# Kernel tuning notes

Hardware: AMD Instinct MI355X
Metric: run time of the kernel (lower is better)

Reference implementation:

```python
import jax, jax.numpy as jnp
import numpy as np


def _delta(x, window):
    # x: [B, T, D]; edge-replicate pad by `window` frames on each side,
    # then weighted antisymmetric finite difference: sum_j (x[t+j]-x[t-j])/(2j).
    B, T, D = x.shape
    pad = jnp.concatenate(
        [jnp.repeat(x[:, :1, :], window, axis=1), x, jnp.repeat(x[:, -1:, :], window, axis=1)],
        axis=1,
    )  # [B, T+2W, D]
    z = jnp.zeros_like(x)
    for j in range(1, window + 1):  # tiny fixed loop over window taps
        z = z + (pad[:, window + j: window + j + T, :] - pad[:, window - j: window - j + T, :]) / (2.0 * j)
    return z


def setup_inputs() -> dict:
    key = jax.random.key(0)
    inp = jax.random.normal(key, (32, 4096, 256), dtype=jnp.float32)
    return {"inp": inp, "window": 2}


def reference(inp, window):
    delta = _delta(inp, window)
    double_delta = _delta(delta, window)
    return jnp.concatenate([inp, delta, double_delta], axis=2)  # [B, T, 3D]
```

## Files before the change

### kernel.cpp

```cpp
#include <hip/hip_runtime.h>


#define TT   4096
#define D4   64
#define O4   192

__device__ __forceinline__ float4 dcomb(const float4 p1, const float4 m1,
                                        const float4 p2, const float4 m2) {
    float4 r;
    r.x = (p1.x - m1.x) * 0.5f + (p2.x - m2.x) * 0.25f;
    r.y = (p1.y - m1.y) * 0.5f + (p2.y - m2.y) * 0.25f;
    r.z = (p1.z - m1.z) * 0.5f + (p2.z - m2.z) * 0.25f;
    r.w = (p1.w - m1.w) * 0.5f + (p2.w - m2.w) * 0.25f;
    return r;
}

__device__ __forceinline__ int clampT(int s) {
    return s < 0 ? 0 : (s > TT - 1 ? TT - 1 : s);
}

__global__ __launch_bounds__(256) void delta_layer_kernel(
        const float* __restrict__ x, float* __restrict__ out) {
    int bid = blockIdx.x;
    int swz = (gridDim.x & 7) == 0
                  ? (bid & 7) * (gridDim.x >> 3) + (bid >> 3)
                  : bid;

    int idx = swz * 256 + (int)threadIdx.x;
    int d4  = idx & (D4 - 1);
    int g   = idx >> 6;
    int t   = g & (TT - 1);
    int b   = g >> 12;

    const float4* xr = reinterpret_cast<const float4*>(x)
                       + (size_t)g * D4 + d4;
    float4* ob = reinterpret_cast<float4*>(out)
                 + (size_t)g * O4 + d4;

    if (t >= 4 && t <= TT - 5) {
        float4 xm4 = xr[-4 * D4];
        float4 xm3 = xr[-3 * D4];
        float4 xm2 = xr[-2 * D4];
        float4 xm1 = xr[-1 * D4];
        float4 x0  = xr[0];
        float4 xp1 = xr[1 * D4];
        float4 xp2 = xr[2 * D4];
        float4 xp3 = xr[3 * D4];
        float4 xp4 = xr[4 * D4];

        float4 dm2 = dcomb(xm1, xm3, x0,  xm4);
        float4 dm1 = dcomb(x0,  xm2, xp1, xm3);
        float4 d0  = dcomb(xp1, xm1, xp2, xm2);
        float4 dp1 = dcomb(xp2, x0,  xp3, xm1);
        float4 dp2 = dcomb(xp3, xp1, xp4, x0);

        ob[0]      = x0;
        ob[D4]     = d0;
        ob[2 * D4] = dcomb(dp1, dm1, dp2, dm2);
    } else {
        const float4* xb = reinterpret_cast<const float4*>(x)
                           + (size_t)b * TT * D4 + d4;
        auto ldc = [&](int r) -> float4 { return xb[clampT(r) * D4]; };
        auto deltaAt = [&](int r) -> float4 {
            return dcomb(ldc(r + 1), ldc(r - 1), ldc(r + 2), ldc(r - 2));
        };
        float4 dm2 = deltaAt(clampT(t - 2));
        float4 dm1 = deltaAt(clampT(t - 1));
        float4 d0  = deltaAt(t);
        float4 dp1 = deltaAt(clampT(t + 1));
        float4 dp2 = deltaAt(clampT(t + 2));

        ob[0]      = ldc(t);
        ob[D4]     = d0;
        ob[2 * D4] = dcomb(dp1, dm1, dp2, dm2);
    }
}

extern "C" void kernel_launch(void* const* d_in, const int* in_sizes, int n_in,
                              void* d_out, int out_size, void* d_ws, size_t ws_size,
                              hipStream_t stream) {
    const float* x = (const float*)d_in[0];
    float* out = (float*)d_out;
    int nthreads = in_sizes[0] / 4;
    int blocks = (nthreads + 255) / 256;
    delta_layer_kernel<<<blocks, 256, 0, stream>>>(x, out);
}
```

Baseline: 515.4 us.

## Stage time-chunk halo tiles in shared memory and use nontemporal stores

Each block now handles a 32-row time chunk of one batch, loading the chunk plus a 4-row halo into LDS once, so the stencil reads come from shared memory rather than nine global reads per output row. Outputs are written with nontemporal stores to avoid polluting the cache with the write-only stream. The cost is an LDS barrier and fewer, larger blocks, with edge chunks still taking the clamped global path.

```diff
diff --git a/kernel.cpp b/kernel.cpp
--- a/kernel.cpp
+++ b/kernel.cpp
@@ -1,9 +1,20 @@
 #include <hip/hip_runtime.h>
 
 
-#define TT   4096
-#define D4   64
-#define O4   192
+#define TT     4096
+#define D4     64
+#define O4     192
+#define TCH    32
+#define NCH    (TT / TCH)
+#define SROWS  (TCH + 8)
+
+typedef float nfloat4 __attribute__((ext_vector_type(4)));
+
+__device__ __forceinline__ void ntstore(const float4 v, float4* p) {
+    union { float4 f; nfloat4 n; } u;
+    u.f = v;
+    __builtin_nontemporal_store(u.n, reinterpret_cast<nfloat4*>(p));
+}
 
 __device__ __forceinline__ float4 dcomb(const float4 p1, const float4 m1,
                                         const float4 p2, const float4 m2) {
@@ -21,58 +32,85 @@
 
 __global__ __launch_bounds__(256) void delta_layer_kernel(
         const float* __restrict__ x, float* __restrict__ out) {
+    __shared__ float4 sh[SROWS * D4];
+
     int bid = blockIdx.x;
     int swz = (gridDim.x & 7) == 0
                   ? (bid & 7) * (gridDim.x >> 3) + (bid >> 3)
                   : bid;
 
-    int idx = swz * 256 + (int)threadIdx.x;
-    int d4  = idx & (D4 - 1);
-    int g   = idx >> 6;
-    int t   = g & (TT - 1);
-    int b   = g >> 12;
+    int ct = swz & (NCH - 1);
+    int b  = swz >> 7;
+    int r0 = ct * TCH;
+    int tid = (int)threadIdx.x;
 
-    const float4* xr = reinterpret_cast<const float4*>(x)
-                       + (size_t)g * D4 + d4;
-    float4* ob = reinterpret_cast<float4*>(out)
-                 + (size_t)g * O4 + d4;
+    const float4* x4 = reinterpret_cast<const float4*>(x);
+    float4* out4 = reinterpret_cast<float4*>(out);
 
-    if (t >= 4 && t <= TT - 5) {
-        float4 xm4 = xr[-4 * D4];
-        float4 xm3 = xr[-3 * D4];
-        float4 xm2 = xr[-2 * D4];
-        float4 xm1 = xr[-1 * D4];
-        float4 x0  = xr[0];
-        float4 xp1 = xr[1 * D4];
-        float4 xp2 = xr[2 * D4];
-        float4 xp3 = xr[3 * D4];
-        float4 xp4 = xr[4 * D4];
+    if (ct >= 1 && ct <= NCH - 2) {
+        const float4* src = x4 + ((size_t)(b * TT + r0 - 4)) * D4;
+        #pragma unroll
+        for (int i = 0; i < SROWS * D4 / 256; ++i) {
+            int s = i * 256 + tid;
+            sh[s] = src[s];
+        }
+        __syncthreads();
 
-        float4 dm2 = dcomb(xm1, xm3, x0,  xm4);
-        float4 dm1 = dcomb(x0,  xm2, xp1, xm3);
-        float4 d0  = dcomb(xp1, xm1, xp2, xm2);
-        float4 dp1 = dcomb(xp2, x0,  xp3, xm1);
-        float4 dp2 = dcomb(xp3, xp1, xp4, x0);
+        #pragma unroll
+        for (int j = 0; j < 8; ++j) {
+            int o    = j * 256 + tid;
+            int trow = o >> 6;
+            int d4   = o & 63;
 
-        ob[0]      = x0;
-        ob[D4]     = d0;
-        ob[2 * D4] = dcomb(dp1, dm1, dp2, dm2);
+            const float4* L = &sh[trow * D4 + d4];
+            float4 xm4 = L[0 * D4];
+            float4 xm3 = L[1 * D4];
+            float4 xm2 = L[2 * D4];
+            float4 xm1 = L[3 * D4];
+            float4 x0  = L[4 * D4];
+            float4 xp1 = L[5 * D4];
+            float4 xp2 = L[6 * D4];
+            float4 xp3 = L[7 * D4];
+            float4 xp4 = L[8 * D4];
+
+            float4 dm2 = dcomb(xm1, xm3, x0,  xm4);
+            float4 dm1 = dcomb(x0,  xm2, xp1, xm3);
+            float4 d0  = dcomb(xp1, xm1, xp2, xm2);
+            float4 dp1 = dcomb(xp2, x0,  xp3, xm1);
+            float4 dp2 = dcomb(xp3, xp1, xp4, x0);
+            float4 dd  = dcomb(dp1, dm1, dp2, dm2);
+
+            float4* ob = out4 + ((size_t)(b * TT + r0 + trow)) * O4 + d4;
+            ntstore(x0, &ob[0]);
+            ntstore(d0, &ob[D4]);
+            ntstore(dd, &ob[2 * D4]);
+        }
     } else {
-        const float4* xb = reinterpret_cast<const float4*>(x)
-                           + (size_t)b * TT * D4 + d4;
-        auto ldc = [&](int r) -> float4 { return xb[clampT(r) * D4]; };
-        auto deltaAt = [&](int r) -> float4 {
-            return dcomb(ldc(r + 1), ldc(r - 1), ldc(r + 2), ldc(r - 2));
-        };
-        float4 dm2 = deltaAt(clampT(t - 2));
-        float4 dm1 = deltaAt(clampT(t - 1));
-        float4 d0  = deltaAt(t);
-        float4 dp1 = deltaAt(clampT(t + 1));
-        float4 dp2 = deltaAt(clampT(t + 2));
+        const float4* xb0 = x4 + (size_t)b * TT * D4;
+        #pragma unroll
+        for (int j = 0; j < 8; ++j) {
+            int o    = j * 256 + tid;
+            int trow = o >> 6;
+            int d4   = o & 63;
+            int t    = r0 + trow;
 
-        ob[0]      = ldc(t);
-        ob[D4]     = d0;
-        ob[2 * D4] = dcomb(dp1, dm1, dp2, dm2);
+            const float4* xb = xb0 + d4;
+            auto ldc = [&](int r) -> float4 { return xb[clampT(r) * D4]; };
+            auto deltaAt = [&](int r) -> float4 {
+                return dcomb(ldc(r + 1), ldc(r - 1), ldc(r + 2), ldc(r - 2));
+            };
+            float4 dm2 = deltaAt(clampT(t - 2));
+            float4 dm1 = deltaAt(clampT(t - 1));
+            float4 d0  = deltaAt(t);
+            float4 dp1 = deltaAt(clampT(t + 1));
+            float4 dp2 = deltaAt(clampT(t + 2));
+            float4 dd  = dcomb(dp1, dm1, dp2, dm2);
+
+            float4* ob = out4 + ((size_t)(b * TT + t)) * O4 + d4;
+            ntstore(ldc(t), &ob[0]);
+            ntstore(d0,     &ob[D4]);
+            ntstore(dd,     &ob[2 * D4]);
+        }
     }
 }
 
@@ -81,7 +119,7 @@
                               hipStream_t stream) {
     const float* x = (const float*)d_in[0];
     float* out = (float*)d_out;
-    int nthreads = in_sizes[0] / 4;
-    int blocks = (nthreads + 255) / 256;
+    int rows = in_sizes[0] / 256;
+    int blocks = rows / TCH;
     delta_layer_kernel<<<blocks, 256, 0, stream>>>(x, out);
 }
```

Measured after the change: 499.4 us. -3.1%, faster.

## Process 8-frame runs per thread with register reuse and nontemporal stores

Applied to the files above, without the earlier changes.

Each thread now computes eight consecutive time frames, loading a 16-frame window into registers once instead of nine loads per output frame. This cuts redundant global and L2 reads of the input. Output writes switch to nontemporal stores so the large output stream does not pollute the cache. The grid shrinks eightfold, which lowers occupancy and raises register pressure per thread.

```diff
diff --git a/kernel.cpp b/kernel.cpp
--- a/kernel.cpp
+++ b/kernel.cpp
@@ -1,9 +1,19 @@
 #include <hip/hip_runtime.h>
 
 
-#define TT   4096
-#define D4   64
-#define O4   192
+#define TT    4096
+#define D4    64
+#define O4    192
+#define WRUN  8
+#define SEGS  (TT / WRUN)
+
+typedef float nfloat4 __attribute__((ext_vector_type(4)));
+
+__device__ __forceinline__ void ntstore(const float4 v, float4* p) {
+    union { float4 f; nfloat4 n; } u;
+    u.f = v;
+    __builtin_nontemporal_store(u.n, reinterpret_cast<nfloat4*>(p));
+}
 
 __device__ __forceinline__ float4 dcomb(const float4 p1, const float4 m1,
                                         const float4 p2, const float4 m2) {
@@ -27,52 +37,55 @@
                   : bid;
 
     int idx = swz * 256 + (int)threadIdx.x;
-    int d4  = idx & (D4 - 1);
-    int g   = idx >> 6;
-    int t   = g & (TT - 1);
-    int b   = g >> 12;
+    int d4  = idx & 63;
+    int seg = idx >> 6;
+    int tb  = seg & (SEGS - 1);
+    int b   = seg >> 9;
+    int w0  = tb * WRUN;
 
-    const float4* xr = reinterpret_cast<const float4*>(x)
-                       + (size_t)g * D4 + d4;
-    float4* ob = reinterpret_cast<float4*>(out)
-                 + (size_t)g * O4 + d4;
+    const float4* x4 = reinterpret_cast<const float4*>(x);
+    float4* out4 = reinterpret_cast<float4*>(out);
 
-    if (t >= 4 && t <= TT - 5) {
-        float4 xm4 = xr[-4 * D4];
-        float4 xm3 = xr[-3 * D4];
-        float4 xm2 = xr[-2 * D4];
-        float4 xm1 = xr[-1 * D4];
-        float4 x0  = xr[0];
-        float4 xp1 = xr[1 * D4];
-        float4 xp2 = xr[2 * D4];
-        float4 xp3 = xr[3 * D4];
-        float4 xp4 = xr[4 * D4];
+    const float4* xr = x4 + ((size_t)(b * TT + w0)) * D4 + d4;
+    float4* ob = out4 + ((size_t)(b * TT + w0)) * O4 + d4;
 
-        float4 dm2 = dcomb(xm1, xm3, x0,  xm4);
-        float4 dm1 = dcomb(x0,  xm2, xp1, xm3);
-        float4 d0  = dcomb(xp1, xm1, xp2, xm2);
-        float4 dp1 = dcomb(xp2, x0,  xp3, xm1);
-        float4 dp2 = dcomb(xp3, xp1, xp4, x0);
+    if (w0 >= 4 && w0 + 11 <= TT - 1) {
+        float4 xq[16];
+        #pragma unroll
+        for (int i = 0; i < 16; ++i) xq[i] = xr[(i - 4) * D4];
 
-        ob[0]      = x0;
-        ob[D4]     = d0;
-        ob[2 * D4] = dcomb(dp1, dm1, dp2, dm2);
+        float4 d[12];
+        #pragma unroll
+        for (int j = 0; j < 12; ++j)
+            d[j] = dcomb(xq[j + 3], xq[j + 1], xq[j + 4], xq[j]);
+
+        #pragma unroll
+        for (int m = 0; m < 8; ++m) {
+            float4 dd = dcomb(d[m + 3], d[m + 1], d[m + 4], d[m]);
+            ntstore(xq[m + 4], &ob[m * O4]);
+            ntstore(d[m + 2],  &ob[m * O4 + D4]);
+            ntstore(dd,        &ob[m * O4 + 2 * D4]);
+        }
     } else {
-        const float4* xb = reinterpret_cast<const float4*>(x)
-                           + (size_t)b * TT * D4 + d4;
+        const float4* xb = x4 + (size_t)b * TT * D4 + d4;
         auto ldc = [&](int r) -> float4 { return xb[clampT(r) * D4]; };
         auto deltaAt = [&](int r) -> float4 {
             return dcomb(ldc(r + 1), ldc(r - 1), ldc(r + 2), ldc(r - 2));
         };
-        float4 dm2 = deltaAt(clampT(t - 2));
-        float4 dm1 = deltaAt(clampT(t - 1));
-        float4 d0  = deltaAt(t);
-        float4 dp1 = deltaAt(clampT(t + 1));
-        float4 dp2 = deltaAt(clampT(t + 2));
+        #pragma unroll
+        for (int m = 0; m < 8; ++m) {
+            int t = w0 + m;
+            float4 dm2 = deltaAt(clampT(t - 2));
+            float4 dm1 = deltaAt(clampT(t - 1));
+            float4 d0  = deltaAt(t);
+            float4 dp1 = deltaAt(clampT(t + 1));
+            float4 dp2 = deltaAt(clampT(t + 2));
+            float4 dd  = dcomb(dp1, dm1, dp2, dm2);
 
-        ob[0]      = ldc(t);
-        ob[D4]     = d0;
-        ob[2 * D4] = dcomb(dp1, dm1, dp2, dm2);
+            ntstore(ldc(t), &ob[m * O4]);
+            ntstore(d0,     &ob[m * O4 + D4]);
+            ntstore(dd,     &ob[m * O4 + 2 * D4]);
+        }
     }
 }
 
@@ -81,7 +94,7 @@
                               hipStream_t stream) {
     const float* x = (const float*)d_in[0];
     float* out = (float*)d_out;
-    int nthreads = in_sizes[0] / 4;
-    int blocks = (nthreads + 255) / 256;
+    int rows = in_sizes[0] / 256;
+    int blocks = rows / 32;
     delta_layer_kernel<<<blocks, 256, 0, stream>>>(x, out);
 }
```

Result: faster. 493.5 us (-4.2%).
